# Optimization experiments

Measured on AMD Instinct MI355X. Metric: run time of the kernel, lower is better.

The kernel has to match this reference:

```python
import jax, jax.numpy as jnp
import numpy as np

B, N, E = 8, 4096, 131072
NODE_DIM, HIDDEN = 64, 128


def _mlp2(x, W1, b1, W2, b2):
    # Linear -> SiLU -> Linear
    return jax.nn.silu(x @ W1 + b1) @ W2 + b2


def setup_inputs() -> dict:
    key = jax.random.key(0)
    ks = jax.random.split(key, 10)
    inp = {
        "node_features": jax.random.normal(ks[0], (B, N, NODE_DIM), jnp.float32),
        "coords": jax.random.normal(ks[1], (B, N, 3), jnp.float32),
        "edge_index": jax.random.randint(ks[2], (2, E), 0, N, jnp.int32),
        # message_net: in = 2*node_dim + 1 = 129
        "Wm1": jax.random.normal(ks[3], (2 * NODE_DIM + 1, HIDDEN), jnp.float32) * 0.05,
        "bm1": jnp.zeros((HIDDEN,), jnp.float32),
        "Wm2": jax.random.normal(ks[4], (HIDDEN, HIDDEN), jnp.float32) * 0.05,
        "bm2": jnp.zeros((HIDDEN,), jnp.float32),
        # node_update: in = node_dim + hidden = 192
        "Wn1": jax.random.normal(ks[5], (NODE_DIM + HIDDEN, HIDDEN), jnp.float32) * 0.05,
        "bn1": jnp.zeros((HIDDEN,), jnp.float32),
        "Wn2": jax.random.normal(ks[6], (HIDDEN, NODE_DIM), jnp.float32) * 0.05,
        "bn2": jnp.zeros((NODE_DIM,), jnp.float32),
        # coord_update: hidden -> hidden -> 1
        "Wc1": jax.random.normal(ks[7], (HIDDEN, HIDDEN), jnp.float32) * 0.05,
        "bc1": jnp.zeros((HIDDEN,), jnp.float32),
        "Wc2": jax.random.normal(ks[8], (HIDDEN, 1), jnp.float32) * 0.05,
        "bc2": jnp.zeros((1,), jnp.float32),
    }
    return inp


def reference(node_features, coords, edge_index, Wm1, bm1, Wm2, bm2,
              Wn1, bn1, Wn2, bn2, Wc1, bc1, Wc2, bc2):
    src, dst = edge_index[0], edge_index[1]
    # Gather per-edge geometry: [B, E, 3]
    edge_vec = coords[:, dst, :] - coords[:, src, :]
    edge_dist = jnp.linalg.norm(edge_vec, axis=-1, keepdims=True)  # [B,E,1]
    edge_vec_n = edge_vec / (edge_dist + 1e-8)
    # Gather node features per edge and build message input: [B, E, 2*D+1]
    msg_in = jnp.concatenate(
        [node_features[:, src, :], node_features[:, dst, :], edge_dist], axis=-1)
    messages = _mlp2(msg_in, Wm1, bm1, Wm2, bm2)  # [B, E, H]
    # Scatter-add messages into destination nodes: [B, N, H]
    agg = jnp.zeros((node_features.shape[0], node_features.shape[1], messages.shape[-1]),
                    dtype=messages.dtype).at[:, dst, :].add(messages)
    # Residual node update
    nf_new = node_features + _mlp2(
        jnp.concatenate([node_features, agg], axis=-1), Wn1, bn1, Wn2, bn2)
    # Equivariant coordinate update
    coord_w = _mlp2(messages, Wc1, bc1, Wc2, bc2)  # [B, E, 1]
    coord_delta = jnp.zeros_like(coords).at[:, dst, :].add(coord_w * edge_vec_n)
    coords_new = coords + coord_delta
    return nf_new, coords_new
```

## Files before the change

### kernel.cpp

```cpp
#include <hip/hip_runtime.h>
#include <hip/hip_bf16.h>

#define B_ 8
#define N_ 4096
#define E_ 131072
#define D_ 64
#define H_ 128

#define EDGE_BLOCKS 256
#define ETILE 128
#define TILES_TOTAL ((B_ * E_) / ETILE)
#define TILES_PER_BLOCK (TILES_TOTAL / EDGE_BLOCKS)

typedef unsigned int u32;
typedef short bf16x8 __attribute__((ext_vector_type(8)));
typedef float f32x4 __attribute__((ext_vector_type(4)));

__device__ __forceinline__ unsigned short f2bf(float f) {
  u32 x = __float_as_uint(f);
  x += 0x7fffu + ((x >> 16) & 1u);
  return (unsigned short)(x >> 16);
}
__device__ __forceinline__ float bf2f(unsigned short v) {
  return __uint_as_float(((u32)v) << 16);
}
__device__ __forceinline__ u32 cvt_pk_bf16(float lo, float hi) {
  u32 r;
  asm("v_cvt_pk_bf16_f32 %0, %1, %2" : "=v"(r) : "v"(lo), "v"(hi));
  return r;
}
__device__ __forceinline__ float silu_f(float x) { return x / (1.0f + __expf(-x)); }

__device__ __forceinline__ int swz(int row, int col) {
  return row * 128 + (col ^ ((row & 7) << 3));
}

#define MFMA(a, b, c) __builtin_amdgcn_mfma_f32_16x16x32_bf16(a, b, c, 0, 0, 0)

__global__ void nf2bf_k(const float* __restrict__ nf, unsigned short* __restrict__ nf16) {
  const int i = blockIdx.x * 256 + threadIdx.x;
  float4 v = ((const float4*)nf)[i];
  u32 p0 = cvt_pk_bf16(v.x, v.y);
  u32 p1 = cvt_pk_bf16(v.z, v.w);
  ((uint2*)nf16)[i] = make_uint2(p0, p1);
}

__global__ void hist_k(const int* __restrict__ ei, int* __restrict__ hist) {
  const int e = blockIdx.x * 256 + threadIdx.x;
  atomicAdd(&hist[ei[E_ + e]], 1);
}

__global__ __launch_bounds__(1024) void scan4096(int* __restrict__ h) {
  __shared__ int wsums[16];
  const int tid = threadIdx.x;
  const int lane = tid & 63, wv = tid >> 6;
  int4 v = ((int4*)h)[tid];
  const int s = v.x + v.y + v.z + v.w;
  int incl = s;
#pragma unroll
  for (int off = 1; off < 64; off <<= 1) {
    int u = __shfl_up(incl, off);
    if (lane >= off) incl += u;
  }
  if (lane == 63) wsums[wv] = incl;
  __syncthreads();
  if (wv == 0) {
    int ws = (lane < 16) ? wsums[lane] : 0;
#pragma unroll
    for (int off = 1; off < 16; off <<= 1) {
      int u = __shfl_up(ws, off);
      if (lane >= off) ws += u;
    }
    if (lane < 16) wsums[lane] = ws;
  }
  __syncthreads();
  int base = (wv ? wsums[wv - 1] : 0) + (incl - s);
  int4 o;
  o.x = base; o.y = base + v.x; o.z = o.y + v.y; o.w = o.z + v.z;
  ((int4*)h)[tid] = o;
}

__global__ void scatter_k(const int* __restrict__ ei, int* __restrict__ offs,
                          int* __restrict__ src_s, int* __restrict__ dst_s) {
  const int e = blockIdx.x * 256 + threadIdx.x;
  const int d = ei[E_ + e];
  const int p = atomicAdd(&offs[d], 1);
  src_s[p] = ei[e];
  dst_s[p] = d;
}

__global__ __launch_bounds__(1024, 4) void egnn_edge_mfma(
    const unsigned short* __restrict__ nf16, const float* __restrict__ coords,
    const int* __restrict__ src_s, const int* __restrict__ dst_s,
    const float* __restrict__ Wm1, const float* __restrict__ bm1,
    const float* __restrict__ Wm2, const float* __restrict__ bm2,
    const float* __restrict__ Wc1, const float* __restrict__ bc1,
    const float* __restrict__ Wc2, const float* __restrict__ bc2,
    float* __restrict__ agg, float* __restrict__ cdelta)
{
  __shared__ unsigned short sW1[128 * 128];
  __shared__ unsigned short sW2[128 * 128];
  __shared__ unsigned short sW3[128 * 128];
  __shared__ unsigned short buf[ETILE * 128];
  __shared__ float4 sgeo[2][ETILE];
  __shared__ int sdst[2][ETILE];
  __shared__ float swpart[4][ETILE];

  const int tid = threadIdx.x;
  for (int i = tid; i < 128 * 128; i += 1024) {
    const int k = i >> 7, n = i & 127;
    const int d = swz(n, k);
    sW1[d] = f2bf(Wm1[i]);
    sW2[d] = f2bf(Wm2[i]);
    sW3[d] = f2bf(Wc1[i]);
  }

  const int lane = tid & 63;
  const int w = tid >> 6;
  const int l15 = lane & 15;
  const int l4 = lane >> 4;
  const int k0l = l4 * 8;
  const int rowbase = (w >> 2) * 32;
  const int colbase = (w & 3) * 32;
  const int rA = rowbase + l15;
  const int rB = colbase + l15;
  const int n0 = colbase + l15;
  const int n1 = n0 + 16;

  const float bb1_0 = bm1[n0], bb1_1 = bm1[n1];
  const float bb2_0 = bm2[n0], bb2_1 = bm2[n1];
  const float bb3_0 = bc1[n0], bb3_1 = bc1[n1];
  const float wc2_0 = Wc2[n0], wc2_1 = Wc2[n1];
  const float wr_0 = Wm1[128 * 128 + n0], wr_1 = Wm1[128 * 128 + n1];
  const float bc2v = bc2[0];

  const int m_t = tid >> 3;
  const int q_t = tid & 7;

  const int myblk = (blockIdx.x & 7) * (EDGE_BLOCKS / 8) + (blockIdx.x >> 3);
  const int b = myblk >> 5;
  const int gbase = (myblk & 31) * TILES_PER_BLOCK;

  __syncthreads();

  for (int t = 0; t < TILES_PER_BLOCK; ++t) {
    const int p = t & 1;
    const int ebase = (gbase + t) * ETILE;

    if (tid < ETILE) {
      const int e = ebase + tid;
      const int s = src_s[e];
      const int d = dst_s[e];
      sdst[p][tid] = d;
      const float* cs = coords + (size_t)(b * N_ + s) * 3;
      const float* cd = coords + (size_t)(b * N_ + d) * 3;
      const float d0 = cd[0] - cs[0], d1 = cd[1] - cs[1], d2 = cd[2] - cs[2];
      const float dist = sqrtf(fmaf(d0, d0, fmaf(d1, d1, d2 * d2)));
      sgeo[p][tid] = make_float4(d0, d1, d2, dist);
    }
    {
      const int e = ebase + m_t;
      const int s = src_s[e];
      const int d = dst_s[e];
      const uint4* ps = (const uint4*)(nf16 + (size_t)(b * N_ + s) * 64);
      const uint4* pd = (const uint4*)(nf16 + (size_t)(b * N_ + d) * 64);
      uint4 vs = ps[q_t];
      uint4 vd = pd[q_t];
      *(uint4*)&buf[swz(m_t, q_t * 8)] = vs;
      *(uint4*)&buf[swz(m_t, 64 + q_t * 8)] = vd;
    }
    __syncthreads();

    f32x4 acc[2][2];
    {
      f32x4 z = {0.f, 0.f, 0.f, 0.f};
      acc[0][0] = z; acc[0][1] = z; acc[1][0] = z; acc[1][1] = z;
    }
#pragma unroll
    for (int ks = 0; ks < 4; ++ks) {
      const int k = ks * 32 + k0l;
      bf16x8 b0 = *(const bf16x8*)&sW1[swz(rB, k)];
      bf16x8 b1 = *(const bf16x8*)&sW1[swz(rB + 16, k)];
      bf16x8 a0 = *(const bf16x8*)&buf[swz(rA, k)];
      bf16x8 a1 = *(const bf16x8*)&buf[swz(rA + 16, k)];
      acc[0][0] = MFMA(a0, b0, acc[0][0]);
      acc[0][1] = MFMA(a0, b1, acc[0][1]);
      acc[1][0] = MFMA(a1, b0, acc[1][0]);
      acc[1][1] = MFMA(a1, b1, acc[1][1]);
    }
    u32 pk[2][4];
#pragma unroll
    for (int i = 0; i < 2; ++i)
#pragma unroll
      for (int r = 0; r < 4; ++r) {
        const int m = rowbase + 16 * i + l4 * 4 + r;
        const float dist = sgeo[p][m].w;
        pk[i][r] = cvt_pk_bf16(silu_f(acc[i][0][r] + bb1_0 + dist * wr_0),
                               silu_f(acc[i][1][r] + bb1_1 + dist * wr_1));
      }
    __syncthreads();
#pragma unroll
    for (int i = 0; i < 2; ++i)
#pragma unroll
      for (int r = 0; r < 4; ++r) {
        const int m = rowbase + 16 * i + l4 * 4 + r;
        buf[swz(m, n0)] = (unsigned short)pk[i][r];
        buf[swz(m, n1)] = (unsigned short)(pk[i][r] >> 16);
      }
    __syncthreads();

    {
      f32x4 z = {0.f, 0.f, 0.f, 0.f};
      acc[0][0] = z; acc[0][1] = z; acc[1][0] = z; acc[1][1] = z;
    }
#pragma unroll
    for (int ks = 0; ks < 4; ++ks) {
      const int k = ks * 32 + k0l;
      bf16x8 b0 = *(const bf16x8*)&sW2[swz(rB, k)];
      bf16x8 b1 = *(const bf16x8*)&sW2[swz(rB + 16, k)];
      bf16x8 a0 = *(const bf16x8*)&buf[swz(rA, k)];
      bf16x8 a1 = *(const bf16x8*)&buf[swz(rA + 16, k)];
      acc[0][0] = MFMA(a0, b0, acc[0][0]);
      acc[0][1] = MFMA(a0, b1, acc[0][1]);
      acc[1][0] = MFMA(a1, b0, acc[1][0]);
      acc[1][1] = MFMA(a1, b1, acc[1][1]);
    }
#pragma unroll
    for (int i = 0; i < 2; ++i)
#pragma unroll
      for (int r = 0; r < 4; ++r)
        pk[i][r] = cvt_pk_bf16(acc[i][0][r] + bb2_0, acc[i][1][r] + bb2_1);
    __syncthreads();
#pragma unroll
    for (int i = 0; i < 2; ++i)
#pragma unroll
      for (int r = 0; r < 4; ++r) {
        const int m = rowbase + 16 * i + l4 * 4 + r;
        buf[swz(m, n0)] = (unsigned short)pk[i][r];
        buf[swz(m, n1)] = (unsigned short)(pk[i][r] >> 16);
      }
    __syncthreads();

    {
      f32x4 z = {0.f, 0.f, 0.f, 0.f};
      acc[0][0] = z; acc[0][1] = z; acc[1][0] = z; acc[1][1] = z;
    }
#pragma unroll
    for (int ks = 0; ks < 4; ++ks) {
      const int k = ks * 32 + k0l;
      bf16x8 b0 = *(const bf16x8*)&sW3[swz(rB, k)];
      bf16x8 b1 = *(const bf16x8*)&sW3[swz(rB + 16, k)];
      bf16x8 a0 = *(const bf16x8*)&buf[swz(rA, k)];
      bf16x8 a1 = *(const bf16x8*)&buf[swz(rA + 16, k)];
      acc[0][0] = MFMA(a0, b0, acc[0][0]);
      acc[0][1] = MFMA(a0, b1, acc[0][1]);
      acc[1][0] = MFMA(a1, b0, acc[1][0]);
      acc[1][1] = MFMA(a1, b1, acc[1][1]);
    }
#pragma unroll
    for (int i = 0; i < 2; ++i)
#pragma unroll
      for (int r = 0; r < 4; ++r) {
        float pw = silu_f(acc[i][0][r] + bb3_0) * wc2_0 +
                   silu_f(acc[i][1][r] + bb3_1) * wc2_1;
        pw += __shfl_xor(pw, 1);
        pw += __shfl_xor(pw, 2);
        pw += __shfl_xor(pw, 4);
        pw += __shfl_xor(pw, 8);
        if (l15 == 0) swpart[w & 3][rowbase + 16 * i + l4 * 4 + r] = pw;
      }

    {
      const int c0 = 2 * (tid & 63);
      int r = (tid >> 6) * 8;
      int cur = sdst[p][r];
      float a0s = 0.f, a1s = 0.f;
#pragma unroll 4
      for (int k = 0; k < 8; ++k, ++r) {
        const int d2 = sdst[p][r];
        if (d2 != cur) {
          float* bp2 = agg + ((size_t)(b * N_ + cur)) * H_ + c0;
          unsafeAtomicAdd(bp2, a0s);
          unsafeAtomicAdd(bp2 + 1, a1s);
          a0s = 0.f; a1s = 0.f;
          cur = d2;
        }
        const u32 pkr = *(const u32*)&buf[swz(r, c0)];
        a0s += bf2f((unsigned short)pkr);
        a1s += bf2f((unsigned short)(pkr >> 16));
      }
      float* bp2 = agg + ((size_t)(b * N_ + cur)) * H_ + c0;
      unsafeAtomicAdd(bp2, a0s);
      unsafeAtomicAdd(bp2 + 1, a1s);
    }
    __syncthreads();

    if (tid < ETILE) {
      float wc = bc2v;
#pragma unroll
      for (int cg = 0; cg < 4; ++cg) wc += swpart[cg][tid];
      const float4 g = sgeo[p][tid];
      const float inv = 1.0f / (g.w + 1e-8f);
      float vx = wc * g.x * inv, vy = wc * g.y * inv, vz = wc * g.z * inv;
      const int myd = sdst[p][tid];
      int flg = (lane == 0) ? 1 : (sdst[p][tid - 1] != myd);
#pragma unroll
      for (int off = 1; off < 64; off <<= 1) {
        float ux = __shfl_up(vx, off);
        float uy = __shfl_up(vy, off);
        float uz = __shfl_up(vz, off);
        int uf = __shfl_up(flg, off);
        if (lane >= off) {
          if (!flg) { vx += ux; vy += uy; vz += uz; }
          flg |= uf;
        }
      }
      const bool tail = (lane == 63) || (sdst[p][tid + 1] != myd);
      if (tail) {
        float* bp = cdelta + ((size_t)(b * N_ + myd)) * 3;
        unsafeAtomicAdd(bp + 0, vx);
        unsafeAtomicAdd(bp + 1, vy);
        unsafeAtomicAdd(bp + 2, vz);
      }
    }
  }
}

#define NTILE 128

__global__ __launch_bounds__(512) void egnn_node_mfma(
    const float* __restrict__ nf, const float* __restrict__ coords,
    const float* __restrict__ agg, const float* __restrict__ cdelta,
    const float* __restrict__ Wn1, const float* __restrict__ bn1,
    const float* __restrict__ Wn2, const float* __restrict__ bn2,
    float* __restrict__ out_nf, float* __restrict__ out_c)
{
  __shared__ unsigned short sA[128 * 192];
  __shared__ unsigned short sB[64 * 128];
  __shared__ unsigned short bufN[128 * 64];
  __shared__ unsigned short bufA[128 * 128];
  __shared__ unsigned short hbuf[128 * 128];

  const int tid = threadIdx.x;
  const int node0 = blockIdx.x * NTILE;

  for (int i = tid; i < 192 * 128; i += 512) {
    const int k = i >> 7, n = i & 127;
    sA[n * 192 + (k ^ ((n & 7) << 3))] = f2bf(Wn1[i]);
  }
  for (int i = tid; i < 128 * 64; i += 512) {
    const int k = i >> 6, n = i & 63;
    sB[n * 128 + (k ^ ((n & 7) << 3))] = f2bf(Wn2[i]);
  }
#pragma unroll
  for (int j = 0; j < 8; ++j) {
    const int p = tid + j * 512;
    const int row = p >> 5, col = 2 * (p & 31);
    float2 v = *(const float2*)&nf[(size_t)(node0 + row) * 64 + col];
    *(u32*)&bufN[row * 64 + (col ^ ((row & 7) << 3))] = cvt_pk_bf16(v.x, v.y);
  }
#pragma unroll
  for (int j = 0; j < 16; ++j) {
    const int p = tid + j * 512;
    const int row = p >> 6, col = 2 * (p & 63);
    float2 v = *(const float2*)&agg[(size_t)(node0 + row) * 128 + col];
    *(u32*)&bufA[row * 128 + (col ^ ((row & 7) << 3))] = cvt_pk_bf16(v.x, v.y);
  }
  if (tid < 3 * NTILE) {
    out_c[(size_t)node0 * 3 + tid] =
        coords[(size_t)node0 * 3 + tid] + cdelta[(size_t)node0 * 3 + tid];
  }

  const int lane = tid & 63;
  const int w = tid >> 6;
  const int l15 = lane & 15;
  const int l4 = lane >> 4;
  const int k0l = l4 * 8;

  const int rb1 = (w & 1) * 64;
  const int cb1 = (w >> 1) * 32;
  const int n0 = cb1 + l15, n1 = n0 + 16;
  const float bb1_0 = bn1[n0], bb1_1 = bn1[n1];

  const int rb2 = (w >> 1) * 32;
  const int cb2 = (w & 1) * 32;
  const int n20 = cb2 + l15, n21 = n20 + 16;
  const float bb2_0 = bn2[n20], bb2_1 = bn2[n21];

  __syncthreads();

  f32x4 acc[4][2];
  {
    f32x4 z = {0.f, 0.f, 0.f, 0.f};
#pragma unroll
    for (int i = 0; i < 4; ++i) { acc[i][0] = z; acc[i][1] = z; }
  }
#pragma unroll
  for (int ks = 0; ks < 2; ++ks) {
    const int k = ks * 32 + k0l;
    bf16x8 b0 = *(const bf16x8*)&sA[n0 * 192 + (k ^ ((n0 & 7) << 3))];
    bf16x8 b1 = *(const bf16x8*)&sA[n1 * 192 + (k ^ ((n1 & 7) << 3))];
#pragma unroll
    for (int i = 0; i < 4; ++i) {
      const int row = rb1 + 16 * i + l15;
      bf16x8 a = *(const bf16x8*)&bufN[row * 64 + (k ^ ((row & 7) << 3))];
      acc[i][0] = MFMA(a, b0, acc[i][0]);
      acc[i][1] = MFMA(a, b1, acc[i][1]);
    }
  }
#pragma unroll
  for (int ks = 0; ks < 4; ++ks) {
    const int k = ks * 32 + k0l;
    const int kg = 64 + k;
    bf16x8 b0 = *(const bf16x8*)&sA[n0 * 192 + (kg ^ ((n0 & 7) << 3))];
    bf16x8 b1 = *(const bf16x8*)&sA[n1 * 192 + (kg ^ ((n1 & 7) << 3))];
#pragma unroll
    for (int i = 0; i < 4; ++i) {
      const int row = rb1 + 16 * i + l15;
      bf16x8 a = *(const bf16x8*)&bufA[row * 128 + (k ^ ((row & 7) << 3))];
      acc[i][0] = MFMA(a, b0, acc[i][0]);
      acc[i][1] = MFMA(a, b1, acc[i][1]);
    }
  }
#pragma unroll
  for (int i = 0; i < 4; ++i)
#pragma unroll
    for (int r = 0; r < 4; ++r) {
      const int m = rb1 + 16 * i + l4 * 4 + r;
      hbuf[m * 128 + (n0 ^ ((m & 7) << 3))] = f2bf(silu_f(acc[i][0][r] + bb1_0));
      hbuf[m * 128 + (n1 ^ ((m & 7) << 3))] = f2bf(silu_f(acc[i][1][r] + bb1_1));
    }
  __syncthreads();

  {
    f32x4 z = {0.f, 0.f, 0.f, 0.f};
    acc[0][0] = z; acc[0][1] = z; acc[1][0] = z; acc[1][1] = z;
  }
#pragma unroll
  for (int ks = 0; ks < 4; ++ks) {
    const int k = ks * 32 + k0l;
    bf16x8 b0 = *(const bf16x8*)&sB[n20 * 128 + (k ^ ((n20 & 7) << 3))];
    bf16x8 b1 = *(const bf16x8*)&sB[n21 * 128 + (k ^ ((n21 & 7) << 3))];
    const int r0 = rb2 + l15, r1 = rb2 + 16 + l15;
    bf16x8 a0 = *(const bf16x8*)&hbuf[r0 * 128 + (k ^ ((r0 & 7) << 3))];
    bf16x8 a1 = *(const bf16x8*)&hbuf[r1 * 128 + (k ^ ((r1 & 7) << 3))];
    acc[0][0] = MFMA(a0, b0, acc[0][0]);
    acc[0][1] = MFMA(a0, b1, acc[0][1]);
    acc[1][0] = MFMA(a1, b0, acc[1][0]);
    acc[1][1] = MFMA(a1, b1, acc[1][1]);
  }
#pragma unroll
  for (int i = 0; i < 2; ++i)
#pragma unroll
    for (int r = 0; r < 4; ++r) {
      const int m = rb2 + 16 * i + l4 * 4 + r;
      const size_t base = (size_t)(node0 + m) * 64;
      out_nf[base + n20] = nf[base + n20] + acc[i][0][r] + bb2_0;
      out_nf[base + n21] = nf[base + n21] + acc[i][1][r] + bb2_1;
    }
}

extern "C" void kernel_launch(void* const* d_in, const int* in_sizes, int n_in,
                              void* d_out, int out_size, void* d_ws, size_t ws_size,
                              hipStream_t stream) {
  const float* nf     = (const float*)d_in[0];
  const float* coords = (const float*)d_in[1];
  const int*   ei     = (const int*)d_in[2];
  const float* Wm1 = (const float*)d_in[3];
  const float* bm1 = (const float*)d_in[4];
  const float* Wm2 = (const float*)d_in[5];
  const float* bm2 = (const float*)d_in[6];
  const float* Wn1 = (const float*)d_in[7];
  const float* bn1 = (const float*)d_in[8];
  const float* Wn2 = (const float*)d_in[9];
  const float* bn2 = (const float*)d_in[10];
  const float* Wc1 = (const float*)d_in[11];
  const float* bc1 = (const float*)d_in[12];
  const float* Wc2 = (const float*)d_in[13];
  const float* bc2 = (const float*)d_in[14];

  float* agg    = (float*)d_ws;
  float* cdelta = agg + (size_t)B_ * N_ * H_;
  int*   hist   = (int*)(cdelta + (size_t)B_ * N_ * 3);
  int*   src_s  = hist + 4096;
  int*   dst_s  = src_s + E_;

  float* out_nf = (float*)d_out;
  float* out_c  = out_nf + (size_t)B_ * N_ * D_;

  unsigned short* nf16 = (unsigned short*)d_out;

  const size_t zero_bytes =
      ((size_t)B_ * N_ * H_ + (size_t)B_ * N_ * 3 + 4096) * sizeof(float);
  hipMemsetAsync(d_ws, 0, zero_bytes, stream);

  nf2bf_k<<<(B_ * N_ * D_ / 4) / 256, 256, 0, stream>>>(nf, nf16);
  hist_k<<<E_ / 256, 256, 0, stream>>>(ei, hist);
  scan4096<<<1, 1024, 0, stream>>>(hist);
  scatter_k<<<E_ / 256, 256, 0, stream>>>(ei, hist, src_s, dst_s);

  egnn_edge_mfma<<<EDGE_BLOCKS, 1024, 0, stream>>>(
      nf16, coords, src_s, dst_s, Wm1, bm1, Wm2, bm2, Wc1, bc1, Wc2, bc2,
      agg, cdelta);
  egnn_node_mfma<<<(B_ * N_) / NTILE, 512, 0, stream>>>(
      nf, coords, agg, cdelta, Wn1, bn1, Wn2, bn2, out_nf, out_c);
}
```

Before: 394.8 us.

## Precompute per-node first-layer projections to remove edge GEMM1

Splits the first message-MLP layer algebraically: node_features @ Wm1[src part] + bm1 and node_features @ Wm1[dst part] are computed once per node in a new kernel (P1, P2), stored as bf16. The edge kernel then gathers 128-wide P1[src] and P2[dst] rows, adds dist*w_r, applies SiLU and goes straight to the second GEMM. This drops one of three per-edge GEMMs and uses separate LDS buffers for the two stages, which removes a pair of barriers. In exchange each edge gathers twice as many bytes (128 instead of 64 bf16 per endpoint), P2 needs extra workspace, and the pre-activation picks up an extra bf16 rounding.

After: 371.9 us (median of 2 runs). 1.06x faster.

```diff
diff --git a/kernel.cpp b/kernel.cpp
--- a/kernel.cpp
+++ b/kernel.cpp
@@ -37,12 +37,73 @@
 
 #define MFMA(a, b, c) __builtin_amdgcn_mfma_f32_16x16x32_bf16(a, b, c, 0, 0, 0)
 
-__global__ void nf2bf_k(const float* __restrict__ nf, unsigned short* __restrict__ nf16) {
-  const int i = blockIdx.x * 256 + threadIdx.x;
-  float4 v = ((const float4*)nf)[i];
-  u32 p0 = cvt_pk_bf16(v.x, v.y);
-  u32 p1 = cvt_pk_bf16(v.z, v.w);
-  ((uint2*)nf16)[i] = make_uint2(p0, p1);
+__global__ __launch_bounds__(512) void p12_k(
+    const float* __restrict__ nf, const float* __restrict__ Wm1,
+    const float* __restrict__ bm1,
+    unsigned short* __restrict__ P1, unsigned short* __restrict__ P2)
+{
+  __shared__ unsigned short sWa[128 * 64];
+  __shared__ unsigned short sWb[128 * 64];
+  __shared__ unsigned short sNf[64 * 64];
+
+  const int tid = threadIdx.x;
+  const int node0 = blockIdx.x * 64;
+
+  for (int i = tid; i < 64 * 128; i += 512) {
+    const int k = i >> 7, n = i & 127;
+    const int d = n * 64 + (k ^ ((n & 7) << 3));
+    sWa[d] = f2bf(Wm1[k * 128 + n]);
+    sWb[d] = f2bf(Wm1[(64 + k) * 128 + n]);
+  }
+  {
+    const int row = tid >> 3, c0 = 8 * (tid & 7);
+    const float4 v0 = *(const float4*)&nf[(size_t)(node0 + row) * 64 + c0];
+    const float4 v1 = *(const float4*)&nf[(size_t)(node0 + row) * 64 + c0 + 4];
+    uint4 pk = make_uint4(cvt_pk_bf16(v0.x, v0.y), cvt_pk_bf16(v0.z, v0.w),
+                          cvt_pk_bf16(v1.x, v1.y), cvt_pk_bf16(v1.z, v1.w));
+    *(uint4*)&sNf[row * 64 + (c0 ^ ((row & 7) << 3))] = pk;
+  }
+  __syncthreads();
+
+  const int lane = tid & 63;
+  const int w = tid >> 6;
+  const int l15 = lane & 15;
+  const int l4 = lane >> 4;
+  const int k0l = l4 * 8;
+  const int colbase = (w & 3) * 32;
+  const int n0 = colbase + l15, n1 = n0 + 16;
+  const unsigned short* sW = (w < 4) ? sWa : sWb;
+  const float add0 = (w < 4) ? bm1[n0] : 0.f;
+  const float add1 = (w < 4) ? bm1[n1] : 0.f;
+  unsigned short* OUT = (w < 4) ? P1 : P2;
+
+  f32x4 acc[4][2];
+  {
+    f32x4 z = {0.f, 0.f, 0.f, 0.f};
+#pragma unroll
+    for (int i = 0; i < 4; ++i) { acc[i][0] = z; acc[i][1] = z; }
+  }
+#pragma unroll
+  for (int ks = 0; ks < 2; ++ks) {
+    const int k = ks * 32 + k0l;
+    bf16x8 b0 = *(const bf16x8*)&sW[n0 * 64 + (k ^ ((n0 & 7) << 3))];
+    bf16x8 b1 = *(const bf16x8*)&sW[n1 * 64 + (k ^ ((n1 & 7) << 3))];
+#pragma unroll
+    for (int i = 0; i < 4; ++i) {
+      const int row = 16 * i + l15;
+      bf16x8 a = *(const bf16x8*)&sNf[row * 64 + (k ^ ((row & 7) << 3))];
+      acc[i][0] = MFMA(a, b0, acc[i][0]);
+      acc[i][1] = MFMA(a, b1, acc[i][1]);
+    }
+  }
+#pragma unroll
+  for (int i = 0; i < 4; ++i)
+#pragma unroll
+    for (int r = 0; r < 4; ++r) {
+      const int m = 16 * i + l4 * 4 + r;
+      OUT[(size_t)(node0 + m) * 128 + n0] = f2bf(acc[i][0][r] + add0);
+      OUT[(size_t)(node0 + m) * 128 + n1] = f2bf(acc[i][1][r] + add1);
+    }
 }
 
 __global__ void hist_k(const int* __restrict__ ei, int* __restrict__ hist) {
@@ -90,18 +151,20 @@
 }
 
 __global__ __launch_bounds__(1024, 4) void egnn_edge_mfma(
-    const unsigned short* __restrict__ nf16, const float* __restrict__ coords,
+    const unsigned short* __restrict__ P1, const unsigned short* __restrict__ P2,
+    const float* __restrict__ coords,
     const int* __restrict__ src_s, const int* __restrict__ dst_s,
-    const float* __restrict__ Wm1, const float* __restrict__ bm1,
+    const float* __restrict__ Wm1,
     const float* __restrict__ Wm2, const float* __restrict__ bm2,
     const float* __restrict__ Wc1, const float* __restrict__ bc1,
     const float* __restrict__ Wc2, const float* __restrict__ bc2,
     float* __restrict__ agg, float* __restrict__ cdelta)
 {
-  __shared__ unsigned short sW1[128 * 128];
   __shared__ unsigned short sW2[128 * 128];
   __shared__ unsigned short sW3[128 * 128];
-  __shared__ unsigned short buf[ETILE * 128];
+  __shared__ unsigned short bufA[ETILE * 128];
+  __shared__ unsigned short bufB[ETILE * 128];
+  __shared__ float swr[128];
   __shared__ float4 sgeo[2][ETILE];
   __shared__ int sdst[2][ETILE];
   __shared__ float swpart[4][ETILE];
@@ -110,10 +173,10 @@
   for (int i = tid; i < 128 * 128; i += 1024) {
     const int k = i >> 7, n = i & 127;
     const int d = swz(n, k);
-    sW1[d] = f2bf(Wm1[i]);
     sW2[d] = f2bf(Wm2[i]);
     sW3[d] = f2bf(Wc1[i]);
   }
+  if (tid < 128) swr[tid] = Wm1[128 * 128 + tid];
 
   const int lane = tid & 63;
   const int w = tid >> 6;
@@ -127,11 +190,9 @@
   const int n0 = colbase + l15;
   const int n1 = n0 + 16;
 
-  const float bb1_0 = bm1[n0], bb1_1 = bm1[n1];
   const float bb2_0 = bm2[n0], bb2_1 = bm2[n1];
   const float bb3_0 = bc1[n0], bb3_1 = bc1[n1];
   const float wc2_0 = Wc2[n0], wc2_1 = Wc2[n1];
-  const float wr_0 = Wm1[128 * 128 + n0], wr_1 = Wm1[128 * 128 + n1];
   const float bc2v = bc2[0];
 
   const int m_t = tid >> 3;
@@ -143,35 +204,51 @@
 
   __syncthreads();
 
+  f32x4 acc[2][2];
+
   for (int t = 0; t < TILES_PER_BLOCK; ++t) {
     const int p = t & 1;
     const int ebase = (gbase + t) * ETILE;
 
-    if (tid < ETILE) {
-      const int e = ebase + tid;
+    {
+      const int e = ebase + m_t;
       const int s = src_s[e];
       const int d = dst_s[e];
-      sdst[p][tid] = d;
       const float* cs = coords + (size_t)(b * N_ + s) * 3;
       const float* cd = coords + (size_t)(b * N_ + d) * 3;
       const float d0 = cd[0] - cs[0], d1 = cd[1] - cs[1], d2 = cd[2] - cs[2];
       const float dist = sqrtf(fmaf(d0, d0, fmaf(d1, d1, d2 * d2)));
-      sgeo[p][tid] = make_float4(d0, d1, d2, dist);
-    }
-    {
-      const int e = ebase + m_t;
-      const int s = src_s[e];
-      const int d = dst_s[e];
-      const uint4* ps = (const uint4*)(nf16 + (size_t)(b * N_ + s) * 64);
-      const uint4* pd = (const uint4*)(nf16 + (size_t)(b * N_ + d) * 64);
-      uint4 vs = ps[q_t];
-      uint4 vd = pd[q_t];
-      *(uint4*)&buf[swz(m_t, q_t * 8)] = vs;
-      *(uint4*)&buf[swz(m_t, 64 + q_t * 8)] = vd;
+      if (q_t == 0) {
+        sdst[p][m_t] = d;
+        sgeo[p][m_t] = make_float4(d0, d1, d2, dist);
+      }
+      const int c0 = 16 * q_t;
+      const uint4* p1p = (const uint4*)(P1 + (size_t)(b * N_ + s) * 128 + c0);
+      const uint4* p2p = (const uint4*)(P2 + (size_t)(b * N_ + d) * 128 + c0);
+      uint4 xa = p1p[0], xb = p1p[1];
+      uint4 ya = p2p[0], yb = p2p[1];
+      u32 opk[8];
+#pragma unroll
+      for (int jj = 0; jj < 4; ++jj) {
+        const float2 wr2 = *(const float2*)&swr[c0 + 2 * jj];
+        const u32 xp = ((const u32*)&xa)[jj], yp = ((const u32*)&ya)[jj];
+        const float lo = bf2f((unsigned short)xp) + bf2f((unsigned short)yp) + dist * wr2.x;
+        const float hi = bf2f((unsigned short)(xp >> 16)) + bf2f((unsigned short)(yp >> 16)) + dist * wr2.y;
+        opk[jj] = cvt_pk_bf16(silu_f(lo), silu_f(hi));
+      }
+#pragma unroll
+      for (int jj = 0; jj < 4; ++jj) {
+        const float2 wr2 = *(const float2*)&swr[c0 + 8 + 2 * jj];
+        const u32 xp = ((const u32*)&xb)[jj], yp = ((const u32*)&yb)[jj];
+        const float lo = bf2f((unsigned short)xp) + bf2f((unsigned short)yp) + dist * wr2.x;
+        const float hi = bf2f((unsigned short)(xp >> 16)) + bf2f((unsigned short)(yp >> 16)) + dist * wr2.y;
+        opk[4 + jj] = cvt_pk_bf16(silu_f(lo), silu_f(hi));
+      }
+      *(uint4*)&bufA[swz(m_t, c0)] = make_uint4(opk[0], opk[1], opk[2], opk[3]);
+      *(uint4*)&bufA[swz(m_t, c0 + 8)] = make_uint4(opk[4], opk[5], opk[6], opk[7]);
     }
     __syncthreads();
 
-    f32x4 acc[2][2];
     {
       f32x4 z = {0.f, 0.f, 0.f, 0.f};
       acc[0][0] = z; acc[0][1] = z; acc[1][0] = z; acc[1][1] = z;
@@ -179,65 +256,23 @@
 #pragma unroll
     for (int ks = 0; ks < 4; ++ks) {
       const int k = ks * 32 + k0l;
-      bf16x8 b0 = *(const bf16x8*)&sW1[swz(rB, k)];
-      bf16x8 b1 = *(const bf16x8*)&sW1[swz(rB + 16, k)];
-      bf16x8 a0 = *(const bf16x8*)&buf[swz(rA, k)];
-      bf16x8 a1 = *(const bf16x8*)&buf[swz(rA + 16, k)];
+      bf16x8 b0 = *(const bf16x8*)&sW2[swz(rB, k)];
+      bf16x8 b1 = *(const bf16x8*)&sW2[swz(rB + 16, k)];
+      bf16x8 a0 = *(const bf16x8*)&bufA[swz(rA, k)];
+      bf16x8 a1 = *(const bf16x8*)&bufA[swz(rA + 16, k)];
       acc[0][0] = MFMA(a0, b0, acc[0][0]);
       acc[0][1] = MFMA(a0, b1, acc[0][1]);
       acc[1][0] = MFMA(a1, b0, acc[1][0]);
       acc[1][1] = MFMA(a1, b1, acc[1][1]);
     }
-    u32 pk[2][4];
 #pragma unroll
     for (int i = 0; i < 2; ++i)
 #pragma unroll
       for (int r = 0; r < 4; ++r) {
         const int m = rowbase + 16 * i + l4 * 4 + r;
-        const float dist = sgeo[p][m].w;
-        pk[i][r] = cvt_pk_bf16(silu_f(acc[i][0][r] + bb1_0 + dist * wr_0),
-                               silu_f(acc[i][1][r] + bb1_1 + dist * wr_1));
-      }
-    __syncthreads();
-#pragma unroll
-    for (int i = 0; i < 2; ++i)
-#pragma unroll
-      for (int r = 0; r < 4; ++r) {
-        const int m = rowbase + 16 * i + l4 * 4 + r;
-        buf[swz(m, n0)] = (unsigned short)pk[i][r];
-        buf[swz(m, n1)] = (unsigned short)(pk[i][r] >> 16);
-      }
-    __syncthreads();
-
-    {
-      f32x4 z = {0.f, 0.f, 0.f, 0.f};
-      acc[0][0] = z; acc[0][1] = z; acc[1][0] = z; acc[1][1] = z;
-    }
-#pragma unroll
-    for (int ks = 0; ks < 4; ++ks) {
-      const int k = ks * 32 + k0l;
-      bf16x8 b0 = *(const bf16x8*)&sW2[swz(rB, k)];
-      bf16x8 b1 = *(const bf16x8*)&sW2[swz(rB + 16, k)];
-      bf16x8 a0 = *(const bf16x8*)&buf[swz(rA, k)];
-      bf16x8 a1 = *(const bf16x8*)&buf[swz(rA + 16, k)];
-      acc[0][0] = MFMA(a0, b0, acc[0][0]);
-      acc[0][1] = MFMA(a0, b1, acc[0][1]);
-      acc[1][0] = MFMA(a1, b0, acc[1][0]);
-      acc[1][1] = MFMA(a1, b1, acc[1][1]);
-    }
-#pragma unroll
-    for (int i = 0; i < 2; ++i)
-#pragma unroll
-      for (int r = 0; r < 4; ++r)
-        pk[i][r] = cvt_pk_bf16(acc[i][0][r] + bb2_0, acc[i][1][r] + bb2_1);
-    __syncthreads();
-#pragma unroll
-    for (int i = 0; i < 2; ++i)
-#pragma unroll
-      for (int r = 0; r < 4; ++r) {
-        const int m = rowbase + 16 * i + l4 * 4 + r;
-        buf[swz(m, n0)] = (unsigned short)pk[i][r];
-        buf[swz(m, n1)] = (unsigned short)(pk[i][r] >> 16);
+        const u32 pk = cvt_pk_bf16(acc[i][0][r] + bb2_0, acc[i][1][r] + bb2_1);
+        bufB[swz(m, n0)] = (unsigned short)pk;
+        bufB[swz(m, n1)] = (unsigned short)(pk >> 16);
       }
     __syncthreads();
 
@@ -250,8 +285,8 @@
       const int k = ks * 32 + k0l;
       bf16x8 b0 = *(const bf16x8*)&sW3[swz(rB, k)];
       bf16x8 b1 = *(const bf16x8*)&sW3[swz(rB + 16, k)];
-      bf16x8 a0 = *(const bf16x8*)&buf[swz(rA, k)];
-      bf16x8 a1 = *(const bf16x8*)&buf[swz(rA + 16, k)];
+      bf16x8 a0 = *(const bf16x8*)&bufB[swz(rA, k)];
+      bf16x8 a1 = *(const bf16x8*)&bufB[swz(rA + 16, k)];
       acc[0][0] = MFMA(a0, b0, acc[0][0]);
       acc[0][1] = MFMA(a0, b1, acc[0][1]);
       acc[1][0] = MFMA(a1, b0, acc[1][0]);
@@ -285,7 +320,7 @@
           a0s = 0.f; a1s = 0.f;
           cur = d2;
         }
-        const u32 pkr = *(const u32*)&buf[swz(r, c0)];
+        const u32 pkr = *(const u32*)&bufB[swz(r, c0)];
         a0s += bf2f((unsigned short)pkr);
         a1s += bf2f((unsigned short)(pkr >> 16));
       }
@@ -484,23 +519,24 @@
   int*   hist   = (int*)(cdelta + (size_t)B_ * N_ * 3);
   int*   src_s  = hist + 4096;
   int*   dst_s  = src_s + E_;
+  unsigned short* P2 = (unsigned short*)(dst_s + E_);
 
   float* out_nf = (float*)d_out;
   float* out_c  = out_nf + (size_t)B_ * N_ * D_;
 
-  unsigned short* nf16 = (unsigned short*)d_out;
+  unsigned short* P1 = (unsigned short*)d_out;
 
   const size_t zero_bytes =
       ((size_t)B_ * N_ * H_ + (size_t)B_ * N_ * 3 + 4096) * sizeof(float);
   hipMemsetAsync(d_ws, 0, zero_bytes, stream);
 
-  nf2bf_k<<<(B_ * N_ * D_ / 4) / 256, 256, 0, stream>>>(nf, nf16);
+  p12_k<<<(B_ * N_) / 64, 512, 0, stream>>>(nf, Wm1, bm1, P1, P2);
   hist_k<<<E_ / 256, 256, 0, stream>>>(ei, hist);
   scan4096<<<1, 1024, 0, stream>>>(hist);
   scatter_k<<<E_ / 256, 256, 0, stream>>>(ei, hist, src_s, dst_s);
 
   egnn_edge_mfma<<<EDGE_BLOCKS, 1024, 0, stream>>>(
-      nf16, coords, src_s, dst_s, Wm1, bm1, Wm2, bm2, Wc1, bc1, Wc2, bc2,
+      P1, P2, coords, src_s, dst_s, Wm1, Wm2, bm2, Wc1, bc1, Wc2, bc2,
       agg, cdelta);
   egnn_node_mfma<<<(B_ * N_) / NTILE, 512, 0, stream>>>(
       nf, coords, agg, cdelta, Wn1, bn1, Wn2, bn2, out_nf, out_c);
```
